# Kernel optimization log

Hardware: AMD Instinct MI355X
Metric: run time of the kernel (lower is better)

The kernel has to match this reference:

```python
import jax, jax.numpy as jnp
import numpy as np

H, D_MODEL, LEN_Q, LEN_K, D_K, D_V = 16, 1024, 512, 2048, 64, 64
B = 4

def setup_inputs() -> dict:
    key = jax.random.key(0)
    ks = jax.random.split(key, 16)
    s = 0.02
    return {
        "Q": jax.random.normal(ks[0], (B, LEN_Q, D_MODEL), jnp.float32),
        "K": jax.random.normal(ks[1], (B, LEN_K, D_MODEL), jnp.float32),
        "V": jax.random.normal(ks[2], (B, LEN_K, D_MODEL), jnp.float32),
        "node_num": LEN_Q,
        "mask": jax.random.randint(ks[3], (B, LEN_K), 0, 2, jnp.int32),
        # params (stored as [in, out] so y = x @ W + b)
        "Wq": jax.random.normal(ks[4], (D_MODEL, H * D_K), jnp.float32) * s,
        "bq": jnp.zeros((H * D_K,), jnp.float32),
        "Wk": jax.random.normal(ks[5], (D_MODEL, H * D_K), jnp.float32) * s,
        "bk": jnp.zeros((H * D_K,), jnp.float32),
        "Wv": jax.random.normal(ks[6], (D_MODEL, H * D_V), jnp.float32) * s,
        "bv": jnp.zeros((H * D_V,), jnp.float32),
        "Wo": jax.random.normal(ks[7], (H * D_V, D_MODEL), jnp.float32) * s,
        "bo": jnp.zeros((D_MODEL,), jnp.float32),
        "gamma": jnp.ones((D_MODEL,), jnp.float32),
        "beta": jnp.zeros((D_MODEL,), jnp.float32),
    }

def _layernorm(x, gamma, beta, eps=1e-5):
    mu = jnp.mean(x, axis=-1, keepdims=True)
    var = jnp.mean((x - mu) ** 2, axis=-1, keepdims=True)
    return (x - mu) * jax.lax.rsqrt(var + eps) * gamma + beta

def reference(Q, K, V, node_num, mask, Wq, bq, Wk, bk, Wv, bv, Wo, bo, gamma, beta):
    b, lq, _ = Q.shape
    lk = K.shape[1]
    q = (Q @ Wq + bq).reshape(b, lq, H, D_K)   # [B, Lq, h, dk]
    k = (K @ Wk + bk).reshape(b, lk, H, D_K)   # [B, Lk, h, dk]
    v = (V @ Wv + bv).reshape(b, lk, H, D_V)   # [B, Lk, h, dv]
    scores = jnp.einsum('bqhd,bkhd->bhqk', q, k) / jnp.sqrt(jnp.float32(D_K))
    scores = jnp.where(mask[:, None, None, :] == 0, -jnp.inf, scores)
    alpha = jax.nn.softmax(scores, axis=-1)    # [B, h, Lq, Lk]
    out = jnp.einsum('bhqk,bkhd->bqhd', alpha, v).reshape(b, lq, H * D_V)
    out = out @ Wo + bo + Q                    # dropout is identity (eval)
    return _layernorm(out, gamma, beta)
```

## Files before the change

kernel.cpp:

```cpp
#include <hip/hip_runtime.h>

typedef __attribute__((ext_vector_type(8))) __bf16 bf16x8;
typedef __attribute__((ext_vector_type(4))) float f32x4;
typedef __attribute__((ext_vector_type(8))) unsigned short u16x8;

__device__ __forceinline__ float bf2f(unsigned short h) {
  union { unsigned int u; float f; } a; a.u = ((unsigned int)h) << 16; return a.f;
}
__device__ __forceinline__ unsigned short f2bf(float f) {
  __bf16 h = (__bf16)f;
  unsigned short u; __builtin_memcpy(&u, &h, 2); return u;
}
__device__ __forceinline__ float fast_exp2(float x) {
#if __has_builtin(__builtin_amdgcn_exp2f)
  return __builtin_amdgcn_exp2f(x);
#else
  return exp2f(x);
#endif
}
__device__ __forceinline__ bf16x8 ld_frag(const unsigned short* p) {
  bf16x8 r; __builtin_memcpy(&r, p, 16); return r;
}
__device__ __forceinline__ void cp16(unsigned short* dst, const unsigned short* src) {
  u16x8 t; __builtin_memcpy(&t, src, 16); __builtin_memcpy(dst, &t, 16);
}

#if __has_builtin(__builtin_amdgcn_global_load_lds)
typedef __attribute__((address_space(3))) unsigned int lds_u32;
typedef const __attribute__((address_space(1))) unsigned int glb_u32;
__device__ __forceinline__ void gload16(const unsigned short* g, unsigned short* l) {
  __builtin_amdgcn_global_load_lds((glb_u32*)g, (lds_u32*)l, 16, 0, 0);
}
#else
__device__ __forceinline__ void gload16(const unsigned short* g, unsigned short* l) {
  cp16(l, g);
}
#endif


__global__ __launch_bounds__(256) void prep_kernel(
    const float* __restrict__ Q, const float* __restrict__ K, const float* __restrict__ V,
    const float* __restrict__ w0, const float* __restrict__ w1,
    const float* __restrict__ w2, const float* __restrict__ w3,
    unsigned short* __restrict__ qb, unsigned short* __restrict__ kb,
    unsigned short* __restrict__ vb, unsigned short* __restrict__ wt)
{
  __shared__ unsigned short tile[64 * 65];
  const int bid = blockIdx.x;
  const int t = threadIdx.x;
  if (bid < 9216) {
    const float* in; unsigned short* out; int i;
    if (bid < 1024)      { in = Q; out = qb; i = bid * 256 + t; }
    else if (bid < 5120) { in = K; out = kb; i = (bid - 1024) * 256 + t; }
    else                 { in = V; out = vb; i = (bid - 5120) * 256 + t; }
    float tf[8]; __builtin_memcpy(tf, &in[(size_t)i * 8], 32);
    unsigned short tu[8];
#pragma unroll
    for (int j = 0; j < 8; j++) tu[j] = f2bf(tf[j]);
    __builtin_memcpy(&out[(size_t)i * 8], tu, 16);
    return;
  }
  const int t4 = bid - 9216;
  const int z = t4 >> 8;
  const float* in = (z == 0) ? w0 : (z == 1) ? w1 : (z == 2) ? w2 : w3;
  unsigned short* o = wt + (size_t)z * 1048576;
  const int dim = 1024;
  const int n0 = (t4 & 15) * 64, k0 = ((t4 >> 4) & 15) * 64;
#pragma unroll
  for (int e = 0; e < 16; e++) {
    int idx = e * 256 + t;
    int i = idx >> 6, j = idx & 63;
    tile[i * 65 + j] = f2bf(in[(size_t)(k0 + i) * dim + n0 + j]);
  }
  __syncthreads();
#pragma unroll
  for (int e = 0; e < 16; e++) {
    int idx = e * 256 + t;
    int i = idx >> 6, j = idx & 63;
    o[(size_t)(n0 + i) * dim + k0 + j] = tile[j * 65 + i];
  }
}

__global__ __launch_bounds__(256, 4) void projqk_kernel(
    const unsigned short* __restrict__ qb,
    const unsigned short* __restrict__ kb,
    const unsigned short* __restrict__ WT4,
    const float* __restrict__ bq, const float* __restrict__ bk,
    unsigned short* __restrict__ qp,
    unsigned short* __restrict__ ktiles)
{
  __shared__ unsigned short pool[18432];
  const int bid = blockIdx.x;
  const int tid  = threadIdx.x;
  const int wave = tid >> 6;
  const int lane = tid & 63;
  const int quad = lane >> 4;
  const int l16  = lane & 15;
  const int K = 1024;
  const f32x4 fz = {0.0f, 0.0f, 0.0f, 0.0f};
  const int srow0 = tid >> 2;
  const int scol  = (tid & 3) * 8;
  const int gcol  = ((tid & 3) ^ ((tid >> 2) & 3)) * 8;
  const int sq    = (quad ^ (l16 & 3)) * 8;
  const int NT = K >> 5;

  if (bid < 512) {
    const int m0 = (bid & 31) * 64;
    const int n0 = (bid >> 5) * 64;
    const int wm = (wave & 1) * 32;
    const int wn = (wave >> 1) * 32;
    f32x4 acc[2][2];
#pragma unroll
    for (int i = 0; i < 2; i++)
#pragma unroll
      for (int j = 0; j < 2; j++) acc[i][j] = fz;

    auto stage = [&](int s, int k0) {
      unsigned short* Asb = pool + s * 2048;
      unsigned short* Bsb = pool + 6144 + s * 2048;
      gload16(&qb[(size_t)(m0 + srow0) * K + k0 + gcol], &Asb[srow0 * 32 + scol]);
      gload16(&WT4[(size_t)(n0 + srow0) * K + k0 + gcol], &Bsb[srow0 * 32 + scol]);
    };
    stage(0, 0);
    stage(1, 32);
    for (int kt = 0; kt < NT; ++kt) {
      if (kt + 1 < NT) asm volatile("s_waitcnt vmcnt(2)" ::: "memory");
      else             asm volatile("s_waitcnt vmcnt(0)" ::: "memory");
      __builtin_amdgcn_s_barrier();
      const int cur = kt % 3;
      const unsigned short* Asb = pool + cur * 2048;
      const unsigned short* Bsb = pool + 6144 + cur * 2048;
      bf16x8 afr[2], bfr[2];
#pragma unroll
      for (int mt = 0; mt < 2; mt++) afr[mt] = ld_frag(&Asb[(wm + mt * 16 + l16) * 32 + sq]);
#pragma unroll
      for (int nt = 0; nt < 2; nt++) bfr[nt] = ld_frag(&Bsb[(wn + nt * 16 + l16) * 32 + sq]);
#pragma unroll
      for (int mt = 0; mt < 2; mt++)
#pragma unroll
        for (int nt = 0; nt < 2; nt++)
          acc[mt][nt] = __builtin_amdgcn_mfma_f32_16x16x32_bf16(afr[mt], bfr[nt], acc[mt][nt], 0, 0, 0);
      if (kt + 2 < NT) stage((kt + 2) % 3, (kt + 2) << 5);
    }
    const float cscale = 0.18033688011112042f;
#pragma unroll
    for (int nt = 0; nt < 2; nt++) {
      int col = n0 + wn + nt * 16 + l16;
      float bsc = bq[col];
#pragma unroll
      for (int mt = 0; mt < 2; mt++) {
        int rowb = m0 + wm + mt * 16 + quad * 4;
#pragma unroll
        for (int r = 0; r < 4; r++)
          qp[(size_t)(rowb + r) * 1024 + col] = f2bf((acc[mt][nt][r] + bsc) * cscale);
      }
    }
  } else {
    const int tb = bid - 512;
    const int m0 = (tb & 63) * 128;
    const int n0 = (tb >> 6) * 64;
    const int wm = (wave & 1) * 64;
    const int wn = (wave >> 1) * 32;
    const unsigned short* BT = WT4 + 1048576;
    f32x4 acc[4][2];
#pragma unroll
    for (int i = 0; i < 4; i++)
#pragma unroll
      for (int j = 0; j < 2; j++) acc[i][j] = fz;

    const int srow1 = srow0 + 64;
    auto stage = [&](int s, int k0) {
      unsigned short* Asb = pool + s * 4096;
      unsigned short* Bsb = pool + 12288 + s * 2048;
      gload16(&kb[(size_t)(m0 + srow0) * K + k0 + gcol], &Asb[srow0 * 32 + scol]);
      gload16(&kb[(size_t)(m0 + srow1) * K + k0 + gcol], &Asb[srow1 * 32 + scol]);
      gload16(&BT[(size_t)(n0 + srow0) * K + k0 + gcol], &Bsb[srow0 * 32 + scol]);
    };
    stage(0, 0);
    stage(1, 32);
    for (int kt = 0; kt < NT; ++kt) {
      if (kt + 1 < NT) asm volatile("s_waitcnt vmcnt(3)" ::: "memory");
      else             asm volatile("s_waitcnt vmcnt(0)" ::: "memory");
      __builtin_amdgcn_s_barrier();
      const int cur = kt % 3;
      const unsigned short* Asb = pool + cur * 4096;
      const unsigned short* Bsb = pool + 12288 + cur * 2048;
      bf16x8 afr[4], bfr[2];
#pragma unroll
      for (int mt = 0; mt < 4; mt++) afr[mt] = ld_frag(&Asb[(wm + mt * 16 + l16) * 32 + sq]);
#pragma unroll
      for (int nt = 0; nt < 2; nt++) bfr[nt] = ld_frag(&Bsb[(wn + nt * 16 + l16) * 32 + sq]);
#pragma unroll
      for (int mt = 0; mt < 4; mt++)
#pragma unroll
        for (int nt = 0; nt < 2; nt++)
          acc[mt][nt] = __builtin_amdgcn_mfma_f32_16x16x32_bf16(afr[mt], bfr[nt], acc[mt][nt], 0, 0, 0);
      if (kt + 2 < NT) stage((kt + 2) % 3, (kt + 2) << 5);
    }
#pragma unroll
    for (int nt = 0; nt < 2; nt++) {
      const int col = n0 + wn + nt * 16 + l16;
      const float bvv = bk[col];
      const int h  = col >> 6;
      const int dk = col & 63;
      const int kc = dk >> 5;
      const int dq = (dk >> 3) & 3;
      const int de = dk & 7;
#pragma unroll
      for (int mt = 0; mt < 4; mt++) {
#pragma unroll
        for (int r = 0; r < 4; r++) {
          const int row = m0 + wm + mt * 16 + quad * 4 + r;
          const int bb = row >> 11, key = row & 2047;
          const size_t tile = ((size_t)((bb * 16 + h) * 32 + (key >> 6))) * 4096;
          const int knt = (key & 63) >> 4;
          const int kl16 = key & 15;
          ktiles[tile + ((size_t)((knt * 2 + kc) * 64 + dq * 16 + kl16)) * 8 + de] =
              f2bf(acc[mt][nt][r] + bvv);
        }
      }
    }
  }
}

__global__ __launch_bounds__(256) void gemm_bt64_kernel(
    const unsigned short* __restrict__ A,
    const unsigned short* __restrict__ BT,
    const float* __restrict__ bias,
    unsigned short* __restrict__ C,
    int M, int N, int K, float cscale)
{
  __shared__ unsigned short pool[12288];
  const int tid  = threadIdx.x;
  const int wave = tid >> 6;
  const int lane = tid & 63;
  const int quad = lane >> 4;
  const int l16  = lane & 15;
  const int m0 = blockIdx.x * 64;
  const int n0 = blockIdx.y * 64;
  const int wm = (wave & 1) * 32;
  const int wn = (wave >> 1) * 32;

  const f32x4 fz = {0.0f, 0.0f, 0.0f, 0.0f};
  f32x4 acc[2][2];
#pragma unroll
  for (int i = 0; i < 2; i++)
#pragma unroll
    for (int j = 0; j < 2; j++) acc[i][j] = fz;

  const int srow0 = tid >> 2;
  const int scol  = (tid & 3) * 8;
  const int gcol  = ((tid & 3) ^ ((tid >> 2) & 3)) * 8;
  const int sq    = (quad ^ (l16 & 3)) * 8;

  auto stage = [&](int s, int k0) {
    unsigned short* Asb = pool + s * 2048;
    unsigned short* Bsb = pool + 6144 + s * 2048;
    gload16(&A[(size_t)(m0 + srow0) * K + k0 + gcol], &Asb[srow0 * 32 + scol]);
    gload16(&BT[(size_t)(n0 + srow0) * K + k0 + gcol], &Bsb[srow0 * 32 + scol]);
  };

  const int NT = K >> 5;
  stage(0, 0);
  stage(1, 32);
  for (int kt = 0; kt < NT; ++kt) {
    if (kt + 1 < NT) asm volatile("s_waitcnt vmcnt(2)" ::: "memory");
    else             asm volatile("s_waitcnt vmcnt(0)" ::: "memory");
    __builtin_amdgcn_s_barrier();
    const int cur = kt % 3;
    const unsigned short* Asb = pool + cur * 2048;
    const unsigned short* Bsb = pool + 6144 + cur * 2048;
    bf16x8 afr[2], bfr[2];
#pragma unroll
    for (int mt = 0; mt < 2; mt++) afr[mt] = ld_frag(&Asb[(wm + mt * 16 + l16) * 32 + sq]);
#pragma unroll
    for (int nt = 0; nt < 2; nt++) bfr[nt] = ld_frag(&Bsb[(wn + nt * 16 + l16) * 32 + sq]);
#pragma unroll
    for (int mt = 0; mt < 2; mt++)
#pragma unroll
      for (int nt = 0; nt < 2; nt++)
        acc[mt][nt] = __builtin_amdgcn_mfma_f32_16x16x32_bf16(afr[mt], bfr[nt], acc[mt][nt], 0, 0, 0);
    if (kt + 2 < NT) stage((kt + 2) % 3, (kt + 2) << 5);
  }

#pragma unroll
  for (int nt = 0; nt < 2; nt++) {
    int col = n0 + wn + nt * 16 + l16;
    float bsc = bias[col];
#pragma unroll
    for (int mt = 0; mt < 2; mt++) {
      int rowb = m0 + wm + mt * 16 + quad * 4;
#pragma unroll
      for (int r = 0; r < 4; r++)
        C[(size_t)(rowb + r) * N + col] = f2bf((acc[mt][nt][r] + bsc) * cscale);
    }
  }
}

__global__ __launch_bounds__(256, 4) void gemm_vt_kernel(
    const unsigned short* __restrict__ A,
    const unsigned short* __restrict__ BT,
    const float* __restrict__ bias,
    unsigned short* __restrict__ vt)
{
  __shared__ unsigned short pool[18432];
  const int K = 1024;
  const int tid  = threadIdx.x;
  const int wave = tid >> 6;
  const int lane = tid & 63;
  const int quad = lane >> 4;
  const int l16  = lane & 15;
  const int m0 = blockIdx.x * 128;
  const int n0 = blockIdx.y * 64;
  const int wm = (wave & 1) * 64;
  const int wn = (wave >> 1) * 32;

  const f32x4 fz = {0.0f, 0.0f, 0.0f, 0.0f};
  f32x4 acc[4][2];
#pragma unroll
  for (int i = 0; i < 4; i++)
#pragma unroll
    for (int j = 0; j < 2; j++) acc[i][j] = fz;

  const int srow0 = tid >> 2;
  const int srow1 = srow0 + 64;
  const int scol  = (tid & 3) * 8;
  const int gcol  = ((tid & 3) ^ ((tid >> 2) & 3)) * 8;
  const int sq    = (quad ^ (l16 & 3)) * 8;

  auto stage = [&](int s, int k0) {
    unsigned short* Asb = pool + s * 4096;
    unsigned short* Bsb = pool + 12288 + s * 2048;
    gload16(&A[(size_t)(m0 + srow0) * K + k0 + gcol], &Asb[srow0 * 32 + scol]);
    gload16(&A[(size_t)(m0 + srow1) * K + k0 + gcol], &Asb[srow1 * 32 + scol]);
    gload16(&BT[(size_t)(n0 + srow0) * K + k0 + gcol], &Bsb[srow0 * 32 + scol]);
  };

  const int NT = K >> 5;
  stage(0, 0);
  stage(1, 32);
  for (int kt = 0; kt < NT; ++kt) {
    if (kt + 1 < NT) asm volatile("s_waitcnt vmcnt(3)" ::: "memory");
    else             asm volatile("s_waitcnt vmcnt(0)" ::: "memory");
    __builtin_amdgcn_s_barrier();
    const int cur = kt % 3;
    const unsigned short* Asb = pool + cur * 4096;
    const unsigned short* Bsb = pool + 12288 + cur * 2048;
    bf16x8 afr[4], bfr[2];
#pragma unroll
    for (int mt = 0; mt < 4; mt++) afr[mt] = ld_frag(&Asb[(wm + mt * 16 + l16) * 32 + sq]);
#pragma unroll
    for (int nt = 0; nt < 2; nt++) bfr[nt] = ld_frag(&Bsb[(wn + nt * 16 + l16) * 32 + sq]);
#pragma unroll
    for (int mt = 0; mt < 4; mt++)
#pragma unroll
      for (int nt = 0; nt < 2; nt++)
        acc[mt][nt] = __builtin_amdgcn_mfma_f32_16x16x32_bf16(afr[mt], bfr[nt], acc[mt][nt], 0, 0, 0);
    if (kt + 2 < NT) stage((kt + 2) % 3, (kt + 2) << 5);
  }
  __syncthreads();

  unsigned short* Ts = pool + wave * 2304;
#pragma unroll
  for (int nt = 0; nt < 2; nt++) {
    const float bvv = bias[n0 + wn + nt * 16 + l16];
#pragma unroll
    for (int mt = 0; mt < 4; mt++)
#pragma unroll
      for (int r = 0; r < 4; r++)
        Ts[(nt * 16 + l16) * 72 + mt * 16 + quad * 4 + r] = f2bf(acc[mt][nt][r] + bvv);
  }
  {
    const int R0 = m0 + wm;
    const int b  = R0 >> 11;
    const int ktile = (R0 & 2047) >> 6;
    const int h = n0 >> 6;
    const int dv_local = lane >> 1;
    const int kc = lane & 1;
    const int dv = wn + dv_local;
    const int dvt = dv >> 4, vl16 = dv & 15;
    const size_t vtile = ((size_t)((b * 16 + h) * 32 + ktile)) * 4096;
#pragma unroll
    for (int jb = 0; jb < 4; jb++) {
      const size_t dst = vtile + ((size_t)((dvt * 2 + kc) * 64 + jb * 16 + vl16)) * 8;
      cp16((unsigned short*)&vt[dst], &Ts[dv_local * 72 + kc * 32 + jb * 8]);
    }
  }
}

__global__ __launch_bounds__(512) void attn_kernel(
    const unsigned short* __restrict__ qp,
    const unsigned short* __restrict__ kp,
    const unsigned short* __restrict__ vt,
    const int* __restrict__ mask,
    unsigned short* __restrict__ attn)
{
  __shared__ unsigned short Kb[3][4096];
  __shared__ unsigned short Vb[3][4096];
  __shared__ int Ms[2048];
  __shared__ unsigned short Ps[8][16 * 72];

  const int tid  = threadIdx.x;
  const int wave = tid >> 6;
  const int lane = tid & 63;
  const int quad = lane >> 4;
  const int l16  = lane & 15;
  const int bid  = blockIdx.x;
  const int bh = bid & 63;
  const int qg = bid >> 6;
  const int b = bh >> 4, h = bh & 15;

  bf16x8 aq[2];
  {
    const size_t qbase = ((size_t)(b * 512 + qg * 128 + wave * 16 + l16)) * 1024 + h * 64;
#pragma unroll
    for (int kc = 0; kc < 2; kc++)
      aq[kc] = ld_frag(&qp[qbase + kc * 32 + quad * 8]);
  }
  {
    const unsigned short* mg = (const unsigned short*)(mask + b * 2048);
    unsigned short* ml = (unsigned short*)Ms;
    gload16(mg + tid * 8, ml + tid * 8);
  }
  asm volatile("s_waitcnt vmcnt(0)" ::: "memory");

  const size_t kvbase = (size_t)bh * 131072;
  auto stageKV = [&](int s, int kt) {
    const unsigned short* ksrc = kp + kvbase + (size_t)kt * 4096;
    const unsigned short* vsrc = vt + kvbase + (size_t)kt * 4096;
    gload16(ksrc + tid * 8, &Kb[s][tid * 8]);
    gload16(vsrc + tid * 8, &Vb[s][tid * 8]);
  };

  const f32x4 fz = {0.0f, 0.0f, 0.0f, 0.0f};
  float l_i[4];
  f32x4 O[4];
#pragma unroll
  for (int r = 0; r < 4; r++) { l_i[r] = 0.0f; O[r] = fz; }

  stageKV(0, 0);
  stageKV(1, 1);
  for (int kt = 0; kt < 32; ++kt) {
    if (kt + 1 < 32) asm volatile("s_waitcnt vmcnt(2)" ::: "memory");
    else             asm volatile("s_waitcnt vmcnt(0)" ::: "memory");
    __builtin_amdgcn_s_barrier();
    const int cur = kt % 3;

    int mk[4];
#pragma unroll
    for (int nt = 0; nt < 4; nt++) mk[nt] = Ms[kt * 64 + nt * 16 + l16];

    f32x4 s[4];
#pragma unroll
    for (int nt = 0; nt < 4; nt++) s[nt] = fz;
    __builtin_amdgcn_s_setprio(1);
#pragma unroll
    for (int nt = 0; nt < 4; nt++)
#pragma unroll
      for (int kc = 0; kc < 2; kc++) {
        bf16x8 bk = ld_frag(&Kb[cur][(nt * 2 + kc) * 512 + lane * 8]);
        s[nt] = __builtin_amdgcn_mfma_f32_16x16x32_bf16(aq[kc], bk, s[nt], 0, 0, 0);
      }
    __builtin_amdgcn_s_setprio(0);

#pragma unroll
    for (int nt = 0; nt < 4; nt++) {
      bool ok = (mk[nt] != 0);
#pragma unroll
      for (int r = 0; r < 4; r++) {
        float p = ok ? fast_exp2(s[nt][r]) : 0.0f;
        l_i[r] += p;
        Ps[wave][(quad * 4 + r) * 72 + nt * 16 + l16] = f2bf(p);
      }
    }

    bf16x8 ap[2];
#pragma unroll
    for (int kc = 0; kc < 2; kc++)
      ap[kc] = ld_frag(&Ps[wave][l16 * 72 + kc * 32 + quad * 8]);
    __builtin_amdgcn_s_setprio(1);
#pragma unroll
    for (int dvt = 0; dvt < 4; dvt++)
#pragma unroll
      for (int kc = 0; kc < 2; kc++) {
        bf16x8 bvf = ld_frag(&Vb[cur][(dvt * 2 + kc) * 512 + lane * 8]);
        O[dvt] = __builtin_amdgcn_mfma_f32_16x16x32_bf16(ap[kc], bvf, O[dvt], 0, 0, 0);
      }
    __builtin_amdgcn_s_setprio(0);
    if (kt + 2 < 32) stageKV((kt + 2) % 3, kt + 2);
  }

#pragma unroll
  for (int off = 1; off < 16; off <<= 1)
#pragma unroll
    for (int r = 0; r < 4; r++) l_i[r] += __shfl_xor(l_i[r], off);

  const int growb = b * 512 + qg * 128 + wave * 16 + quad * 4;
#pragma unroll
  for (int r = 0; r < 4; r++) {
    const float inv = (l_i[r] > 0.0f) ? (1.0f / l_i[r]) : 0.0f;
#pragma unroll
    for (int dvt = 0; dvt < 4; dvt++)
      attn[(size_t)(growb + r) * 1024 + h * 64 + dvt * 16 + l16] = f2bf(O[dvt][r] * inv);
  }
}

__global__ __launch_bounds__(256) void ln_kernel(
    const unsigned short* __restrict__ x,
    const float* __restrict__ resid,
    const float* __restrict__ gamma,
    const float* __restrict__ beta,
    float* __restrict__ out)
{
  const int row = blockIdx.x;
  const int t = threadIdx.x;
  const int wave = t >> 6, lane = t & 63;
  __shared__ float red[8];
  float v[4];
  float s1 = 0.0f, s2 = 0.0f;
#pragma unroll
  for (int i = 0; i < 4; i++) {
    int e = t + i * 256;
    float val = bf2f(x[(size_t)row * 1024 + e]) + resid[(size_t)row * 1024 + e];
    v[i] = val; s1 += val; s2 += val * val;
  }
#pragma unroll
  for (int off = 1; off < 64; off <<= 1) { s1 += __shfl_xor(s1, off); s2 += __shfl_xor(s2, off); }
  if (lane == 0) { red[wave] = s1; red[4 + wave] = s2; }
  __syncthreads();
  s1 = red[0] + red[1] + red[2] + red[3];
  s2 = red[4] + red[5] + red[6] + red[7];
  float mu  = s1 * (1.0f / 1024.0f);
  float var = s2 * (1.0f / 1024.0f) - mu * mu;
  float rstd = rsqrtf(var + 1e-5f);
#pragma unroll
  for (int i = 0; i < 4; i++) {
    int e = t + i * 256;
    out[(size_t)row * 1024 + e] = (v[i] - mu) * rstd * gamma[e] + beta[e];
  }
}

extern "C" void kernel_launch(void* const* d_in, const int* in_sizes, int n_in,
                              void* d_out, int out_size, void* d_ws, size_t ws_size,
                              hipStream_t stream) {
  (void)out_size; (void)ws_size;
  const float* Q = (const float*)d_in[0];
  const float* K = (const float*)d_in[1];
  const float* V = (const float*)d_in[2];

  int ix = 3;
  if (ix < n_in && in_sizes[ix] == 1) ix++;
  const int* mask  = (const int*)d_in[ix++];
  const float* Wq = (const float*)d_in[ix++]; const float* bq = (const float*)d_in[ix++];
  const float* Wk = (const float*)d_in[ix++]; const float* bk = (const float*)d_in[ix++];
  const float* Wv = (const float*)d_in[ix++]; const float* bv = (const float*)d_in[ix++];
  const float* Wo = (const float*)d_in[ix++]; const float* bo = (const float*)d_in[ix++];
  const float* gm = (const float*)d_in[ix++]; const float* bt = (const float*)d_in[ix++];

  char* ws = (char*)d_ws;
  dim3 blk(256);
  dim3 blk512(512);

  unsigned short* WT4    = (unsigned short*)(ws);
  unsigned short* qp     = (unsigned short*)(ws + (8ull  << 20));
  unsigned short* kb     = (unsigned short*)(ws + (12ull << 20));
  unsigned short* vtiles = kb;
  unsigned short* vb     = (unsigned short*)(ws + (28ull << 20));
  unsigned short* qb     = (unsigned short*)(ws + (44ull << 20));
  unsigned short* at     = qb;
  unsigned short* ktiles = (unsigned short*)(ws + (48ull << 20));

  prep_kernel<<<dim3(10240), blk, 0, stream>>>(Q, K, V, Wq, Wk, Wv, Wo, qb, kb, vb, WT4);
  projqk_kernel<<<dim3(1536), blk, 0, stream>>>(qb, kb, WT4, bq, bk, qp, ktiles);
  gemm_vt_kernel<<<dim3(64, 16), blk, 0, stream>>>(vb, WT4 + 2097152, bv, vtiles);
  attn_kernel<<<dim3(256), blk512, 0, stream>>>(qp, ktiles, vtiles, mask, at);
  gemm_bt64_kernel<<<dim3(32, 16), blk, 0, stream>>>(at, WT4 + 3145728, bo, qp, 2048, 1024, 1024, 1.0f);
  ln_kernel<<<dim3(2048), blk, 0, stream>>>(qp, Q, gm, bt, (float*)d_out);
}
```

Baseline: 259.9 us.

## Fuse fp32-to-bf16 activation conversion into projection GEMM loads and merge V projection

Drops the separate pass that converts Q, K and V from fp32 to bf16. The projection GEMMs now load fp32 activations into registers, convert them and store bf16 into LDS, while the weight tile still uses direct global-to-LDS loads. The V projection is merged into the same launch as the Q and K projections. This removes a full write and reread of the bf16 activation copies and one kernel launch, in exchange for register-staged loads, more VGPR pressure, and loss of the XOR swizzle on LDS fragment reads, which may cause bank conflicts.

```diff
diff --git a/kernel.cpp b/kernel.cpp
--- a/kernel.cpp
+++ b/kernel.cpp
@@ -37,30 +37,14 @@
 }
 #endif
 
-
 __global__ __launch_bounds__(256) void prep_kernel(
-    const float* __restrict__ Q, const float* __restrict__ K, const float* __restrict__ V,
     const float* __restrict__ w0, const float* __restrict__ w1,
     const float* __restrict__ w2, const float* __restrict__ w3,
-    unsigned short* __restrict__ qb, unsigned short* __restrict__ kb,
-    unsigned short* __restrict__ vb, unsigned short* __restrict__ wt)
+    unsigned short* __restrict__ wt)
 {
   __shared__ unsigned short tile[64 * 65];
-  const int bid = blockIdx.x;
+  const int t4 = blockIdx.x;
   const int t = threadIdx.x;
-  if (bid < 9216) {
-    const float* in; unsigned short* out; int i;
-    if (bid < 1024)      { in = Q; out = qb; i = bid * 256 + t; }
-    else if (bid < 5120) { in = K; out = kb; i = (bid - 1024) * 256 + t; }
-    else                 { in = V; out = vb; i = (bid - 5120) * 256 + t; }
-    float tf[8]; __builtin_memcpy(tf, &in[(size_t)i * 8], 32);
-    unsigned short tu[8];
-#pragma unroll
-    for (int j = 0; j < 8; j++) tu[j] = f2bf(tf[j]);
-    __builtin_memcpy(&out[(size_t)i * 8], tu, 16);
-    return;
-  }
-  const int t4 = bid - 9216;
   const int z = t4 >> 8;
   const float* in = (z == 0) ? w0 : (z == 1) ? w1 : (z == 2) ? w2 : w3;
   unsigned short* o = wt + (size_t)z * 1048576;
@@ -81,13 +65,13 @@
   }
 }
 
-__global__ __launch_bounds__(256, 4) void projqk_kernel(
-    const unsigned short* __restrict__ qb,
-    const unsigned short* __restrict__ kb,
+__global__ __launch_bounds__(256, 4) void proj_kernel(
+    const float* __restrict__ Qf, const float* __restrict__ Kf, const float* __restrict__ Vf,
     const unsigned short* __restrict__ WT4,
-    const float* __restrict__ bq, const float* __restrict__ bk,
+    const float* __restrict__ bq, const float* __restrict__ bk, const float* __restrict__ bv,
     unsigned short* __restrict__ qp,
-    unsigned short* __restrict__ ktiles)
+    unsigned short* __restrict__ ktiles,
+    unsigned short* __restrict__ vtiles)
 {
   __shared__ unsigned short pool[18432];
   const int bid = blockIdx.x;
@@ -96,108 +80,131 @@
   const int lane = tid & 63;
   const int quad = lane >> 4;
   const int l16  = lane & 15;
-  const int K = 1024;
+  const int KD = 1024, NT = 32;
   const f32x4 fz = {0.0f, 0.0f, 0.0f, 0.0f};
   const int srow0 = tid >> 2;
   const int scol  = (tid & 3) * 8;
-  const int gcol  = ((tid & 3) ^ ((tid >> 2) & 3)) * 8;
-  const int sq    = (quad ^ (l16 & 3)) * 8;
-  const int NT = K >> 5;
+
+#define Q_ISSUE(kt, X0, X1) do { \
+    const int k0_ = (kt) << 5; \
+    gload16(&BT[(size_t)(n0 + srow0) * KD + k0_ + scol], &pool[6144 + ((kt) % 3) * 2048 + srow0 * 32 + scol]); \
+    __builtin_memcpy(&X0, &Qf[(size_t)(m0 + srow0) * KD + k0_ + scol], 16); \
+    __builtin_memcpy(&X1, &Qf[(size_t)(m0 + srow0) * KD + k0_ + scol + 4], 16); \
+  } while (0)
+#define Q_COMMIT(slot, X0, X1) do { \
+    unsigned short tu_[8]; \
+    for (int j_ = 0; j_ < 4; j_++) { tu_[j_] = f2bf(X0[j_]); tu_[4 + j_] = f2bf(X1[j_]); } \
+    __builtin_memcpy(&pool[(slot) * 2048 + srow0 * 32 + scol], tu_, 16); \
+  } while (0)
+#define Q_COMP(kt) do { \
+    const unsigned short* Asb_ = pool + ((kt) % 3) * 2048; \
+    const unsigned short* Bsb_ = pool + 6144 + ((kt) % 3) * 2048; \
+    bf16x8 afr_[2], bfr_[2]; \
+    for (int mt_ = 0; mt_ < 2; mt_++) afr_[mt_] = ld_frag(&Asb_[(wm + mt_ * 16 + l16) * 32 + quad * 8]); \
+    for (int nt_ = 0; nt_ < 2; nt_++) bfr_[nt_] = ld_frag(&Bsb_[(wn + nt_ * 16 + l16) * 32 + quad * 8]); \
+    for (int mt_ = 0; mt_ < 2; mt_++) \
+      for (int nt_ = 0; nt_ < 2; nt_++) \
+        acc[mt_][nt_] = __builtin_amdgcn_mfma_f32_16x16x32_bf16(afr_[mt_], bfr_[nt_], acc[mt_][nt_], 0, 0, 0); \
+  } while (0)
+#define Q_ITER(kt, I0, I1, C0, C1) do { \
+    __builtin_amdgcn_s_barrier(); \
+    Q_COMP(kt); \
+    if ((kt) + 2 < NT) Q_ISSUE((kt) + 2, I0, I1); \
+    if ((kt) + 1 < NT) { \
+      if ((kt) + 2 < NT) { asm volatile("s_waitcnt vmcnt(3)" ::: "memory"); } \
+      else               { asm volatile("s_waitcnt vmcnt(0)" ::: "memory"); } \
+      Q_COMMIT(((kt) + 1) % 3, C0, C1); \
+      asm volatile("s_waitcnt lgkmcnt(0)" ::: "memory"); \
+    } \
+  } while (0)
+
+#define KV_ISSUE(AP, kt, X0, X1, X2, X3) do { \
+    const int k0_ = (kt) << 5; \
+    gload16(&BT[(size_t)(n0 + srow0) * KD + k0_ + scol], &pool[12288 + ((kt) % 3) * 2048 + srow0 * 32 + scol]); \
+    __builtin_memcpy(&X0, &AP[(size_t)(m0 + srow0) * KD + k0_ + scol], 16); \
+    __builtin_memcpy(&X1, &AP[(size_t)(m0 + srow0) * KD + k0_ + scol + 4], 16); \
+    __builtin_memcpy(&X2, &AP[(size_t)(m0 + srow1) * KD + k0_ + scol], 16); \
+    __builtin_memcpy(&X3, &AP[(size_t)(m0 + srow1) * KD + k0_ + scol + 4], 16); \
+  } while (0)
+#define KV_COMMIT(slot, X0, X1, X2, X3) do { \
+    unsigned short tu_[8]; \
+    for (int j_ = 0; j_ < 4; j_++) { tu_[j_] = f2bf(X0[j_]); tu_[4 + j_] = f2bf(X1[j_]); } \
+    __builtin_memcpy(&pool[(slot) * 4096 + srow0 * 32 + scol], tu_, 16); \
+    for (int j_ = 0; j_ < 4; j_++) { tu_[j_] = f2bf(X2[j_]); tu_[4 + j_] = f2bf(X3[j_]); } \
+    __builtin_memcpy(&pool[(slot) * 4096 + srow1 * 32 + scol], tu_, 16); \
+  } while (0)
+#define KV_COMP(kt) do { \
+    const unsigned short* Asb_ = pool + ((kt) % 3) * 4096; \
+    const unsigned short* Bsb_ = pool + 12288 + ((kt) % 3) * 2048; \
+    bf16x8 afr_[4], bfr_[2]; \
+    for (int mt_ = 0; mt_ < 4; mt_++) afr_[mt_] = ld_frag(&Asb_[(wm + mt_ * 16 + l16) * 32 + quad * 8]); \
+    for (int nt_ = 0; nt_ < 2; nt_++) bfr_[nt_] = ld_frag(&Bsb_[(wn + nt_ * 16 + l16) * 32 + quad * 8]); \
+    for (int mt_ = 0; mt_ < 4; mt_++) \
+      for (int nt_ = 0; nt_ < 2; nt_++) \
+        acc[mt_][nt_] = __builtin_amdgcn_mfma_f32_16x16x32_bf16(afr_[mt_], bfr_[nt_], acc[mt_][nt_], 0, 0, 0); \
+  } while (0)
+#define KV_ITER(AP, kt, I0, I1, I2, I3, C0, C1, C2, C3) do { \
+    __builtin_amdgcn_s_barrier(); \
+    KV_COMP(kt); \
+    if ((kt) + 2 < NT) KV_ISSUE(AP, (kt) + 2, I0, I1, I2, I3); \
+    if ((kt) + 1 < NT) { \
+      if ((kt) + 2 < NT) { asm volatile("s_waitcnt vmcnt(5)" ::: "memory"); } \
+      else               { asm volatile("s_waitcnt vmcnt(0)" ::: "memory"); } \
+      KV_COMMIT(((kt) + 1) % 3, C0, C1, C2, C3); \
+      asm volatile("s_waitcnt lgkmcnt(0)" ::: "memory"); \
+    } \
+  } while (0)
 
   if (bid < 512) {
     const int m0 = (bid & 31) * 64;
     const int n0 = (bid >> 5) * 64;
     const int wm = (wave & 1) * 32;
     const int wn = (wave >> 1) * 32;
+    const unsigned short* BT = WT4;
     f32x4 acc[2][2];
-#pragma unroll
     for (int i = 0; i < 2; i++)
-#pragma unroll
       for (int j = 0; j < 2; j++) acc[i][j] = fz;
-
-    auto stage = [&](int s, int k0) {
-      unsigned short* Asb = pool + s * 2048;
-      unsigned short* Bsb = pool + 6144 + s * 2048;
-      gload16(&qb[(size_t)(m0 + srow0) * K + k0 + gcol], &Asb[srow0 * 32 + scol]);
-      gload16(&WT4[(size_t)(n0 + srow0) * K + k0 + gcol], &Bsb[srow0 * 32 + scol]);
-    };
-    stage(0, 0);
-    stage(1, 32);
-    for (int kt = 0; kt < NT; ++kt) {
-      if (kt + 1 < NT) asm volatile("s_waitcnt vmcnt(2)" ::: "memory");
-      else             asm volatile("s_waitcnt vmcnt(0)" ::: "memory");
-      __builtin_amdgcn_s_barrier();
-      const int cur = kt % 3;
-      const unsigned short* Asb = pool + cur * 2048;
-      const unsigned short* Bsb = pool + 6144 + cur * 2048;
-      bf16x8 afr[2], bfr[2];
-#pragma unroll
-      for (int mt = 0; mt < 2; mt++) afr[mt] = ld_frag(&Asb[(wm + mt * 16 + l16) * 32 + sq]);
-#pragma unroll
-      for (int nt = 0; nt < 2; nt++) bfr[nt] = ld_frag(&Bsb[(wn + nt * 16 + l16) * 32 + sq]);
-#pragma unroll
-      for (int mt = 0; mt < 2; mt++)
-#pragma unroll
-        for (int nt = 0; nt < 2; nt++)
-          acc[mt][nt] = __builtin_amdgcn_mfma_f32_16x16x32_bf16(afr[mt], bfr[nt], acc[mt][nt], 0, 0, 0);
-      if (kt + 2 < NT) stage((kt + 2) % 3, (kt + 2) << 5);
+    f32x4 qa0, qa1, qb0, qb1;
+    Q_ISSUE(0, qa0, qa1);
+    Q_ISSUE(1, qb0, qb1);
+    asm volatile("s_waitcnt vmcnt(3)" ::: "memory");
+    Q_COMMIT(0, qa0, qa1);
+    asm volatile("s_waitcnt lgkmcnt(0)" ::: "memory");
+    for (int kt = 0; kt < NT; kt += 2) {
+      Q_ITER(kt,     qa0, qa1, qb0, qb1);
+      Q_ITER(kt + 1, qb0, qb1, qa0, qa1);
     }
     const float cscale = 0.18033688011112042f;
-#pragma unroll
     for (int nt = 0; nt < 2; nt++) {
       int col = n0 + wn + nt * 16 + l16;
       float bsc = bq[col];
-#pragma unroll
       for (int mt = 0; mt < 2; mt++) {
         int rowb = m0 + wm + mt * 16 + quad * 4;
-#pragma unroll
         for (int r = 0; r < 4; r++)
           qp[(size_t)(rowb + r) * 1024 + col] = f2bf((acc[mt][nt][r] + bsc) * cscale);
       }
     }
-  } else {
+  } else if (bid < 1536) {
     const int tb = bid - 512;
     const int m0 = (tb & 63) * 128;
     const int n0 = (tb >> 6) * 64;
     const int wm = (wave & 1) * 64;
     const int wn = (wave >> 1) * 32;
+    const int srow1 = srow0 + 64;
     const unsigned short* BT = WT4 + 1048576;
     f32x4 acc[4][2];
-#pragma unroll
     for (int i = 0; i < 4; i++)
-#pragma unroll
       for (int j = 0; j < 2; j++) acc[i][j] = fz;
-
-    const int srow1 = srow0 + 64;
-    auto stage = [&](int s, int k0) {
-      unsigned short* Asb = pool + s * 4096;
-      unsigned short* Bsb = pool + 12288 + s * 2048;
-      gload16(&kb[(size_t)(m0 + srow0) * K + k0 + gcol], &Asb[srow0 * 32 + scol]);
-      gload16(&kb[(size_t)(m0 + srow1) * K + k0 + gcol], &Asb[srow1 * 32 + scol]);
-      gload16(&BT[(size_t)(n0 + srow0) * K + k0 + gcol], &Bsb[srow0 * 32 + scol]);
-    };
-    stage(0, 0);
-    stage(1, 32);
-    for (int kt = 0; kt < NT; ++kt) {
-      if (kt + 1 < NT) asm volatile("s_waitcnt vmcnt(3)" ::: "memory");
-      else             asm volatile("s_waitcnt vmcnt(0)" ::: "memory");
-      __builtin_amdgcn_s_barrier();
-      const int cur = kt % 3;
-      const unsigned short* Asb = pool + cur * 4096;
-      const unsigned short* Bsb = pool + 12288 + cur * 2048;
-      bf16x8 afr[4], bfr[2];
-#pragma unroll
-      for (int mt = 0; mt < 4; mt++) afr[mt] = ld_frag(&Asb[(wm + mt * 16 + l16) * 32 + sq]);
-#pragma unroll
-      for (int nt = 0; nt < 2; nt++) bfr[nt] = ld_frag(&Bsb[(wn + nt * 16 + l16) * 32 + sq]);
-#pragma unroll
-      for (int mt = 0; mt < 4; mt++)
-#pragma unroll
-        for (int nt = 0; nt < 2; nt++)
-          acc[mt][nt] = __builtin_amdgcn_mfma_f32_16x16x32_bf16(afr[mt], bfr[nt], acc[mt][nt], 0, 0, 0);
-      if (kt + 2 < NT) stage((kt + 2) % 3, (kt + 2) << 5);
-    }
-#pragma unroll
+    f32x4 ka0, ka1, ka2, ka3, kb0, kb1, kb2, kb3;
+    KV_ISSUE(Kf, 0, ka0, ka1, ka2, ka3);
+    KV_ISSUE(Kf, 1, kb0, kb1, kb2, kb3);
+    asm volatile("s_waitcnt vmcnt(5)" ::: "memory");
+    KV_COMMIT(0, ka0, ka1, ka2, ka3);
+    asm volatile("s_waitcnt lgkmcnt(0)" ::: "memory");
+    for (int kt = 0; kt < NT; kt += 2) {
+      KV_ITER(Kf, kt,     ka0, ka1, ka2, ka3, kb0, kb1, kb2, kb3);
+      KV_ITER(Kf, kt + 1, kb0, kb1, kb2, kb3, ka0, ka1, ka2, ka3);
+    }
     for (int nt = 0; nt < 2; nt++) {
       const int col = n0 + wn + nt * 16 + l16;
       const float bvv = bk[col];
@@ -206,9 +213,7 @@
       const int kc = dk >> 5;
       const int dq = (dk >> 3) & 3;
       const int de = dk & 7;
-#pragma unroll
       for (int mt = 0; mt < 4; mt++) {
-#pragma unroll
         for (int r = 0; r < 4; r++) {
           const int row = m0 + wm + mt * 16 + quad * 4 + r;
           const int bb = row >> 11, key = row & 2047;
@@ -220,7 +225,60 @@
         }
       }
     }
-  }
+  } else {
+    const int tb = bid - 1536;
+    const int m0 = (tb & 63) * 128;
+    const int n0 = (tb >> 6) * 64;
+    const int wm = (wave & 1) * 64;
+    const int wn = (wave >> 1) * 32;
+    const int srow1 = srow0 + 64;
+    const unsigned short* BT = WT4 + 2097152;
+    f32x4 acc[4][2];
+    for (int i = 0; i < 4; i++)
+      for (int j = 0; j < 2; j++) acc[i][j] = fz;
+    f32x4 va0, va1, va2, va3, vb0, vb1, vb2, vb3;
+    KV_ISSUE(Vf, 0, va0, va1, va2, va3);
+    KV_ISSUE(Vf, 1, vb0, vb1, vb2, vb3);
+    asm volatile("s_waitcnt vmcnt(5)" ::: "memory");
+    KV_COMMIT(0, va0, va1, va2, va3);
+    asm volatile("s_waitcnt lgkmcnt(0)" ::: "memory");
+    for (int kt = 0; kt < NT; kt += 2) {
+      KV_ITER(Vf, kt,     va0, va1, va2, va3, vb0, vb1, vb2, vb3);
+      KV_ITER(Vf, kt + 1, vb0, vb1, vb2, vb3, va0, va1, va2, va3);
+    }
+    __syncthreads();
+
+    unsigned short* Ts = pool + wave * 2304;
+    for (int nt = 0; nt < 2; nt++) {
+      const float bvv = bv[n0 + wn + nt * 16 + l16];
+      for (int mt = 0; mt < 4; mt++)
+        for (int r = 0; r < 4; r++)
+          Ts[(nt * 16 + l16) * 72 + mt * 16 + quad * 4 + r] = f2bf(acc[mt][nt][r] + bvv);
+    }
+    {
+      const int R0 = m0 + wm;
+      const int b  = R0 >> 11;
+      const int ktile = (R0 & 2047) >> 6;
+      const int h = n0 >> 6;
+      const int dv_local = lane >> 1;
+      const int kc = lane & 1;
+      const int dv = wn + dv_local;
+      const int dvt = dv >> 4, vl16 = dv & 15;
+      const size_t vtile = ((size_t)((b * 16 + h) * 32 + ktile)) * 4096;
+      for (int jb = 0; jb < 4; jb++) {
+        const size_t dst = vtile + ((size_t)((dvt * 2 + kc) * 64 + jb * 16 + vl16)) * 8;
+        cp16((unsigned short*)&vtiles[dst], &Ts[dv_local * 72 + kc * 32 + jb * 8]);
+      }
+    }
+  }
+#undef Q_ISSUE
+#undef Q_COMMIT
+#undef Q_COMP
+#undef Q_ITER
+#undef KV_ISSUE
+#undef KV_COMMIT
+#undef KV_COMP
+#undef KV_ITER
 }
 
 __global__ __launch_bounds__(256) void gemm_bt64_kernel(
@@ -297,97 +355,6 @@
   }
 }
 
-__global__ __launch_bounds__(256, 4) void gemm_vt_kernel(
-    const unsigned short* __restrict__ A,
-    const unsigned short* __restrict__ BT,
-    const float* __restrict__ bias,
-    unsigned short* __restrict__ vt)
-{
-  __shared__ unsigned short pool[18432];
-  const int K = 1024;
-  const int tid  = threadIdx.x;
-  const int wave = tid >> 6;
-  const int lane = tid & 63;
-  const int quad = lane >> 4;
-  const int l16  = lane & 15;
-  const int m0 = blockIdx.x * 128;
-  const int n0 = blockIdx.y * 64;
-  const int wm = (wave & 1) * 64;
-  const int wn = (wave >> 1) * 32;
-
-  const f32x4 fz = {0.0f, 0.0f, 0.0f, 0.0f};
-  f32x4 acc[4][2];
-#pragma unroll
-  for (int i = 0; i < 4; i++)
-#pragma unroll
-    for (int j = 0; j < 2; j++) acc[i][j] = fz;
-
-  const int srow0 = tid >> 2;
-  const int srow1 = srow0 + 64;
-  const int scol  = (tid & 3) * 8;
-  const int gcol  = ((tid & 3) ^ ((tid >> 2) & 3)) * 8;
-  const int sq    = (quad ^ (l16 & 3)) * 8;
-
-  auto stage = [&](int s, int k0) {
-    unsigned short* Asb = pool + s * 4096;
-    unsigned short* Bsb = pool + 12288 + s * 2048;
-    gload16(&A[(size_t)(m0 + srow0) * K + k0 + gcol], &Asb[srow0 * 32 + scol]);
-    gload16(&A[(size_t)(m0 + srow1) * K + k0 + gcol], &Asb[srow1 * 32 + scol]);
-    gload16(&BT[(size_t)(n0 + srow0) * K + k0 + gcol], &Bsb[srow0 * 32 + scol]);
-  };
-
-  const int NT = K >> 5;
-  stage(0, 0);
-  stage(1, 32);
-  for (int kt = 0; kt < NT; ++kt) {
-    if (kt + 1 < NT) asm volatile("s_waitcnt vmcnt(3)" ::: "memory");
-    else             asm volatile("s_waitcnt vmcnt(0)" ::: "memory");
-    __builtin_amdgcn_s_barrier();
-    const int cur = kt % 3;
-    const unsigned short* Asb = pool + cur * 4096;
-    const unsigned short* Bsb = pool + 12288 + cur * 2048;
-    bf16x8 afr[4], bfr[2];
-#pragma unroll
-    for (int mt = 0; mt < 4; mt++) afr[mt] = ld_frag(&Asb[(wm + mt * 16 + l16) * 32 + sq]);
-#pragma unroll
-    for (int nt = 0; nt < 2; nt++) bfr[nt] = ld_frag(&Bsb[(wn + nt * 16 + l16) * 32 + sq]);
-#pragma unroll
-    for (int mt = 0; mt < 4; mt++)
-#pragma unroll
-      for (int nt = 0; nt < 2; nt++)
-        acc[mt][nt] = __builtin_amdgcn_mfma_f32_16x16x32_bf16(afr[mt], bfr[nt], acc[mt][nt], 0, 0, 0);
-    if (kt + 2 < NT) stage((kt + 2) % 3, (kt + 2) << 5);
-  }
-  __syncthreads();
-
-  unsigned short* Ts = pool + wave * 2304;
-#pragma unroll
-  for (int nt = 0; nt < 2; nt++) {
-    const float bvv = bias[n0 + wn + nt * 16 + l16];
-#pragma unroll
-    for (int mt = 0; mt < 4; mt++)
-#pragma unroll
-      for (int r = 0; r < 4; r++)
-        Ts[(nt * 16 + l16) * 72 + mt * 16 + quad * 4 + r] = f2bf(acc[mt][nt][r] + bvv);
-  }
-  {
-    const int R0 = m0 + wm;
-    const int b  = R0 >> 11;
-    const int ktile = (R0 & 2047) >> 6;
-    const int h = n0 >> 6;
-    const int dv_local = lane >> 1;
-    const int kc = lane & 1;
-    const int dv = wn + dv_local;
-    const int dvt = dv >> 4, vl16 = dv & 15;
-    const size_t vtile = ((size_t)((b * 16 + h) * 32 + ktile)) * 4096;
-#pragma unroll
-    for (int jb = 0; jb < 4; jb++) {
-      const size_t dst = vtile + ((size_t)((dvt * 2 + kc) * 64 + jb * 16 + vl16)) * 8;
-      cp16((unsigned short*)&vt[dst], &Ts[dv_local * 72 + kc * 32 + jb * 8]);
-    }
-  }
-}
-
 __global__ __launch_bounds__(512) void attn_kernel(
     const unsigned short* __restrict__ qp,
     const unsigned short* __restrict__ kp,
@@ -563,16 +530,12 @@
 
   unsigned short* WT4    = (unsigned short*)(ws);
   unsigned short* qp     = (unsigned short*)(ws + (8ull  << 20));
-  unsigned short* kb     = (unsigned short*)(ws + (12ull << 20));
-  unsigned short* vtiles = kb;
-  unsigned short* vb     = (unsigned short*)(ws + (28ull << 20));
-  unsigned short* qb     = (unsigned short*)(ws + (44ull << 20));
-  unsigned short* at     = qb;
-  unsigned short* ktiles = (unsigned short*)(ws + (48ull << 20));
-
-  prep_kernel<<<dim3(10240), blk, 0, stream>>>(Q, K, V, Wq, Wk, Wv, Wo, qb, kb, vb, WT4);
-  projqk_kernel<<<dim3(1536), blk, 0, stream>>>(qb, kb, WT4, bq, bk, qp, ktiles);
-  gemm_vt_kernel<<<dim3(64, 16), blk, 0, stream>>>(vb, WT4 + 2097152, bv, vtiles);
+  unsigned short* ktiles = (unsigned short*)(ws + (12ull << 20));
+  unsigned short* vtiles = (unsigned short*)(ws + (28ull << 20));
+  unsigned short* at     = (unsigned short*)(ws + (44ull << 20));
+
+  prep_kernel<<<dim3(1024), blk, 0, stream>>>(Wq, Wk, Wv, Wo, WT4);
+  proj_kernel<<<dim3(2560), blk, 0, stream>>>(Q, K, V, WT4, bq, bk, bv, qp, ktiles, vtiles);
   attn_kernel<<<dim3(256), blk512, 0, stream>>>(qp, ktiles, vtiles, mask, at);
   gemm_bt64_kernel<<<dim3(32, 16), blk, 0, stream>>>(at, WT4 + 3145728, bo, qp, 2048, 1024, 1024, 1.0f);
   ln_kernel<<<dim3(2048), blk, 0, stream>>>(qp, Q, gm, bt, (float*)d_out);
```

After: 275.6 us. +6.1%, slower.

## Give each wave private LDS staging to drop block barriers in projection GEMMs

Applied to the files above, without the earlier changes.

The Q/K projection and V projection GEMMs now have each wave load its own A and B sub-tiles into a private LDS region, so the per-iteration block-wide s_barrier is removed and each wave waits only on its own vmcnt. This removes cross-wave synchronisation stalls in the k-loop. The cost is duplicated global loads, since waves sharing rows or columns each fetch them, plus doubled LDS per block, which lowers the occupancy hint from 4 to 2. The XOR swizzle is also dropped, so LDS bank conflicts may increase.

```diff
diff --git a/kernel.cpp b/kernel.cpp
--- a/kernel.cpp
+++ b/kernel.cpp
@@ -36,7 +36,6 @@
   cp16(l, g);
 }
 #endif
-
 
 __global__ __launch_bounds__(256) void prep_kernel(
     const float* __restrict__ Q, const float* __restrict__ K, const float* __restrict__ V,
@@ -81,7 +80,7 @@
   }
 }
 
-__global__ __launch_bounds__(256, 4) void projqk_kernel(
+__global__ __launch_bounds__(256, 2) void projqk_kernel(
     const unsigned short* __restrict__ qb,
     const unsigned short* __restrict__ kb,
     const unsigned short* __restrict__ WT4,
@@ -89,20 +88,18 @@
     unsigned short* __restrict__ qp,
     unsigned short* __restrict__ ktiles)
 {
-  __shared__ unsigned short pool[18432];
+  __shared__ unsigned short pool[36864];
   const int bid = blockIdx.x;
   const int tid  = threadIdx.x;
   const int wave = tid >> 6;
   const int lane = tid & 63;
   const int quad = lane >> 4;
   const int l16  = lane & 15;
-  const int K = 1024;
+  const int KD = 1024, NT = 32;
   const f32x4 fz = {0.0f, 0.0f, 0.0f, 0.0f};
-  const int srow0 = tid >> 2;
-  const int scol  = (tid & 3) * 8;
-  const int gcol  = ((tid & 3) ^ ((tid >> 2) & 3)) * 8;
-  const int sq    = (quad ^ (l16 & 3)) * 8;
-  const int NT = K >> 5;
+  const int wbase = wave * 9216;
+  const int r0 = lane >> 2;
+  const int c0 = (lane & 3) * 8;
 
   if (bid < 512) {
     const int m0 = (bid & 31) * 64;
@@ -116,25 +113,25 @@
       for (int j = 0; j < 2; j++) acc[i][j] = fz;
 
     auto stage = [&](int s, int k0) {
-      unsigned short* Asb = pool + s * 2048;
-      unsigned short* Bsb = pool + 6144 + s * 2048;
-      gload16(&qb[(size_t)(m0 + srow0) * K + k0 + gcol], &Asb[srow0 * 32 + scol]);
-      gload16(&WT4[(size_t)(n0 + srow0) * K + k0 + gcol], &Bsb[srow0 * 32 + scol]);
+      unsigned short* wA = pool + wbase + s * 2048;
+      unsigned short* wB = wA + 1024;
+      gload16(&qb[(size_t)(m0 + wm + r0) * KD + k0 + c0],       wA + lane * 8);
+      gload16(&qb[(size_t)(m0 + wm + 16 + r0) * KD + k0 + c0],  wA + 512 + lane * 8);
+      gload16(&WT4[(size_t)(n0 + wn + r0) * KD + k0 + c0],      wB + lane * 8);
+      gload16(&WT4[(size_t)(n0 + wn + 16 + r0) * KD + k0 + c0], wB + 512 + lane * 8);
     };
     stage(0, 0);
     stage(1, 32);
     for (int kt = 0; kt < NT; ++kt) {
-      if (kt + 1 < NT) asm volatile("s_waitcnt vmcnt(2)" ::: "memory");
+      if (kt + 1 < NT) asm volatile("s_waitcnt vmcnt(4)" ::: "memory");
       else             asm volatile("s_waitcnt vmcnt(0)" ::: "memory");
-      __builtin_amdgcn_s_barrier();
-      const int cur = kt % 3;
-      const unsigned short* Asb = pool + cur * 2048;
-      const unsigned short* Bsb = pool + 6144 + cur * 2048;
+      const unsigned short* wA = pool + wbase + (kt % 3) * 2048;
+      const unsigned short* wB = wA + 1024;
       bf16x8 afr[2], bfr[2];
 #pragma unroll
-      for (int mt = 0; mt < 2; mt++) afr[mt] = ld_frag(&Asb[(wm + mt * 16 + l16) * 32 + sq]);
-#pragma unroll
-      for (int nt = 0; nt < 2; nt++) bfr[nt] = ld_frag(&Bsb[(wn + nt * 16 + l16) * 32 + sq]);
+      for (int mt = 0; mt < 2; mt++) afr[mt] = ld_frag(&wA[(mt * 16 + l16) * 32 + quad * 8]);
+#pragma unroll
+      for (int nt = 0; nt < 2; nt++) bfr[nt] = ld_frag(&wB[(nt * 16 + l16) * 32 + quad * 8]);
 #pragma unroll
       for (int mt = 0; mt < 2; mt++)
 #pragma unroll
@@ -168,28 +165,28 @@
 #pragma unroll
       for (int j = 0; j < 2; j++) acc[i][j] = fz;
 
-    const int srow1 = srow0 + 64;
     auto stage = [&](int s, int k0) {
-      unsigned short* Asb = pool + s * 4096;
-      unsigned short* Bsb = pool + 12288 + s * 2048;
-      gload16(&kb[(size_t)(m0 + srow0) * K + k0 + gcol], &Asb[srow0 * 32 + scol]);
-      gload16(&kb[(size_t)(m0 + srow1) * K + k0 + gcol], &Asb[srow1 * 32 + scol]);
-      gload16(&BT[(size_t)(n0 + srow0) * K + k0 + gcol], &Bsb[srow0 * 32 + scol]);
+      unsigned short* wA = pool + wbase + s * 3072;
+      unsigned short* wB = wA + 2048;
+      gload16(&kb[(size_t)(m0 + wm + r0) * KD + k0 + c0],       wA + lane * 8);
+      gload16(&kb[(size_t)(m0 + wm + 16 + r0) * KD + k0 + c0],  wA + 512 + lane * 8);
+      gload16(&kb[(size_t)(m0 + wm + 32 + r0) * KD + k0 + c0],  wA + 1024 + lane * 8);
+      gload16(&kb[(size_t)(m0 + wm + 48 + r0) * KD + k0 + c0],  wA + 1536 + lane * 8);
+      gload16(&BT[(size_t)(n0 + wn + r0) * KD + k0 + c0],       wB + lane * 8);
+      gload16(&BT[(size_t)(n0 + wn + 16 + r0) * KD + k0 + c0],  wB + 512 + lane * 8);
     };
     stage(0, 0);
     stage(1, 32);
     for (int kt = 0; kt < NT; ++kt) {
-      if (kt + 1 < NT) asm volatile("s_waitcnt vmcnt(3)" ::: "memory");
+      if (kt + 1 < NT) asm volatile("s_waitcnt vmcnt(6)" ::: "memory");
       else             asm volatile("s_waitcnt vmcnt(0)" ::: "memory");
-      __builtin_amdgcn_s_barrier();
-      const int cur = kt % 3;
-      const unsigned short* Asb = pool + cur * 4096;
-      const unsigned short* Bsb = pool + 12288 + cur * 2048;
+      const unsigned short* wA = pool + wbase + (kt % 3) * 3072;
+      const unsigned short* wB = wA + 2048;
       bf16x8 afr[4], bfr[2];
 #pragma unroll
-      for (int mt = 0; mt < 4; mt++) afr[mt] = ld_frag(&Asb[(wm + mt * 16 + l16) * 32 + sq]);
-#pragma unroll
-      for (int nt = 0; nt < 2; nt++) bfr[nt] = ld_frag(&Bsb[(wn + nt * 16 + l16) * 32 + sq]);
+      for (int mt = 0; mt < 4; mt++) afr[mt] = ld_frag(&wA[(mt * 16 + l16) * 32 + quad * 8]);
+#pragma unroll
+      for (int nt = 0; nt < 2; nt++) bfr[nt] = ld_frag(&wB[(nt * 16 + l16) * 32 + quad * 8]);
 #pragma unroll
       for (int mt = 0; mt < 4; mt++)
 #pragma unroll
@@ -219,6 +216,92 @@
               f2bf(acc[mt][nt][r] + bvv);
         }
       }
+    }
+  }
+}
+
+__global__ __launch_bounds__(256, 2) void gemm_vt_kernel(
+    const unsigned short* __restrict__ A,
+    const unsigned short* __restrict__ BT,
+    const float* __restrict__ bias,
+    unsigned short* __restrict__ vt)
+{
+  __shared__ unsigned short pool[36864];
+  const int KD = 1024, NT = 32;
+  const int tid  = threadIdx.x;
+  const int wave = tid >> 6;
+  const int lane = tid & 63;
+  const int quad = lane >> 4;
+  const int l16  = lane & 15;
+  const int m0 = blockIdx.x * 128;
+  const int n0 = blockIdx.y * 64;
+  const int wm = (wave & 1) * 64;
+  const int wn = (wave >> 1) * 32;
+  const int wbase = wave * 9216;
+  const int r0 = lane >> 2;
+  const int c0 = (lane & 3) * 8;
+
+  const f32x4 fz = {0.0f, 0.0f, 0.0f, 0.0f};
+  f32x4 acc[4][2];
+#pragma unroll
+  for (int i = 0; i < 4; i++)
+#pragma unroll
+    for (int j = 0; j < 2; j++) acc[i][j] = fz;
+
+  auto stage = [&](int s, int k0) {
+    unsigned short* wA = pool + wbase + s * 3072;
+    unsigned short* wB = wA + 2048;
+    gload16(&A[(size_t)(m0 + wm + r0) * KD + k0 + c0],       wA + lane * 8);
+    gload16(&A[(size_t)(m0 + wm + 16 + r0) * KD + k0 + c0],  wA + 512 + lane * 8);
+    gload16(&A[(size_t)(m0 + wm + 32 + r0) * KD + k0 + c0],  wA + 1024 + lane * 8);
+    gload16(&A[(size_t)(m0 + wm + 48 + r0) * KD + k0 + c0],  wA + 1536 + lane * 8);
+    gload16(&BT[(size_t)(n0 + wn + r0) * KD + k0 + c0],      wB + lane * 8);
+    gload16(&BT[(size_t)(n0 + wn + 16 + r0) * KD + k0 + c0], wB + 512 + lane * 8);
+  };
+  stage(0, 0);
+  stage(1, 32);
+  for (int kt = 0; kt < NT; ++kt) {
+    if (kt + 1 < NT) asm volatile("s_waitcnt vmcnt(6)" ::: "memory");
+    else             asm volatile("s_waitcnt vmcnt(0)" ::: "memory");
+    const unsigned short* wA = pool + wbase + (kt % 3) * 3072;
+    const unsigned short* wB = wA + 2048;
+    bf16x8 afr[4], bfr[2];
+#pragma unroll
+    for (int mt = 0; mt < 4; mt++) afr[mt] = ld_frag(&wA[(mt * 16 + l16) * 32 + quad * 8]);
+#pragma unroll
+    for (int nt = 0; nt < 2; nt++) bfr[nt] = ld_frag(&wB[(nt * 16 + l16) * 32 + quad * 8]);
+#pragma unroll
+    for (int mt = 0; mt < 4; mt++)
+#pragma unroll
+      for (int nt = 0; nt < 2; nt++)
+        acc[mt][nt] = __builtin_amdgcn_mfma_f32_16x16x32_bf16(afr[mt], bfr[nt], acc[mt][nt], 0, 0, 0);
+    if (kt + 2 < NT) stage((kt + 2) % 3, (kt + 2) << 5);
+  }
+  asm volatile("s_waitcnt lgkmcnt(0)" ::: "memory");
+  unsigned short* Ts = pool + wbase;
+#pragma unroll
+  for (int nt = 0; nt < 2; nt++) {
+    const float bvv = bias[n0 + wn + nt * 16 + l16];
+#pragma unroll
+    for (int mt = 0; mt < 4; mt++)
+#pragma unroll
+      for (int r = 0; r < 4; r++)
+        Ts[(nt * 16 + l16) * 72 + mt * 16 + quad * 4 + r] = f2bf(acc[mt][nt][r] + bvv);
+  }
+  {
+    const int R0 = m0 + wm;
+    const int b  = R0 >> 11;
+    const int ktile = (R0 & 2047) >> 6;
+    const int h = n0 >> 6;
+    const int dv_local = lane >> 1;
+    const int kc = lane & 1;
+    const int dv = wn + dv_local;
+    const int dvt = dv >> 4, vl16 = dv & 15;
+    const size_t vtile = ((size_t)((b * 16 + h) * 32 + ktile)) * 4096;
+#pragma unroll
+    for (int jb = 0; jb < 4; jb++) {
+      const size_t dst = vtile + ((size_t)((dvt * 2 + kc) * 64 + jb * 16 + vl16)) * 8;
+      cp16((unsigned short*)&vt[dst], &Ts[dv_local * 72 + kc * 32 + jb * 8]);
     }
   }
 }
@@ -297,97 +380,6 @@
   }
 }
 
-__global__ __launch_bounds__(256, 4) void gemm_vt_kernel(
-    const unsigned short* __restrict__ A,
-    const unsigned short* __restrict__ BT,
-    const float* __restrict__ bias,
-    unsigned short* __restrict__ vt)
-{
-  __shared__ unsigned short pool[18432];
-  const int K = 1024;
-  const int tid  = threadIdx.x;
-  const int wave = tid >> 6;
-  const int lane = tid & 63;
-  const int quad = lane >> 4;
-  const int l16  = lane & 15;
-  const int m0 = blockIdx.x * 128;
-  const int n0 = blockIdx.y * 64;
-  const int wm = (wave & 1) * 64;
-  const int wn = (wave >> 1) * 32;
-
-  const f32x4 fz = {0.0f, 0.0f, 0.0f, 0.0f};
-  f32x4 acc[4][2];
-#pragma unroll
-  for (int i = 0; i < 4; i++)
-#pragma unroll
-    for (int j = 0; j < 2; j++) acc[i][j] = fz;
-
-  const int srow0 = tid >> 2;
-  const int srow1 = srow0 + 64;
-  const int scol  = (tid & 3) * 8;
-  const int gcol  = ((tid & 3) ^ ((tid >> 2) & 3)) * 8;
-  const int sq    = (quad ^ (l16 & 3)) * 8;
-
-  auto stage = [&](int s, int k0) {
-    unsigned short* Asb = pool + s * 4096;
-    unsigned short* Bsb = pool + 12288 + s * 2048;
-    gload16(&A[(size_t)(m0 + srow0) * K + k0 + gcol], &Asb[srow0 * 32 + scol]);
-    gload16(&A[(size_t)(m0 + srow1) * K + k0 + gcol], &Asb[srow1 * 32 + scol]);
-    gload16(&BT[(size_t)(n0 + srow0) * K + k0 + gcol], &Bsb[srow0 * 32 + scol]);
-  };
-
-  const int NT = K >> 5;
-  stage(0, 0);
-  stage(1, 32);
-  for (int kt = 0; kt < NT; ++kt) {
-    if (kt + 1 < NT) asm volatile("s_waitcnt vmcnt(3)" ::: "memory");
-    else             asm volatile("s_waitcnt vmcnt(0)" ::: "memory");
-    __builtin_amdgcn_s_barrier();
-    const int cur = kt % 3;
-    const unsigned short* Asb = pool + cur * 4096;
-    const unsigned short* Bsb = pool + 12288 + cur * 2048;
-    bf16x8 afr[4], bfr[2];
-#pragma unroll
-    for (int mt = 0; mt < 4; mt++) afr[mt] = ld_frag(&Asb[(wm + mt * 16 + l16) * 32 + sq]);
-#pragma unroll
-    for (int nt = 0; nt < 2; nt++) bfr[nt] = ld_frag(&Bsb[(wn + nt * 16 + l16) * 32 + sq]);
-#pragma unroll
-    for (int mt = 0; mt < 4; mt++)
-#pragma unroll
-      for (int nt = 0; nt < 2; nt++)
-        acc[mt][nt] = __builtin_amdgcn_mfma_f32_16x16x32_bf16(afr[mt], bfr[nt], acc[mt][nt], 0, 0, 0);
-    if (kt + 2 < NT) stage((kt + 2) % 3, (kt + 2) << 5);
-  }
-  __syncthreads();
-
-  unsigned short* Ts = pool + wave * 2304;
-#pragma unroll
-  for (int nt = 0; nt < 2; nt++) {
-    const float bvv = bias[n0 + wn + nt * 16 + l16];
-#pragma unroll
-    for (int mt = 0; mt < 4; mt++)
-#pragma unroll
-      for (int r = 0; r < 4; r++)
-        Ts[(nt * 16 + l16) * 72 + mt * 16 + quad * 4 + r] = f2bf(acc[mt][nt][r] + bvv);
-  }
-  {
-    const int R0 = m0 + wm;
-    const int b  = R0 >> 11;
-    const int ktile = (R0 & 2047) >> 6;
-    const int h = n0 >> 6;
-    const int dv_local = lane >> 1;
-    const int kc = lane & 1;
-    const int dv = wn + dv_local;
-    const int dvt = dv >> 4, vl16 = dv & 15;
-    const size_t vtile = ((size_t)((b * 16 + h) * 32 + ktile)) * 4096;
-#pragma unroll
-    for (int jb = 0; jb < 4; jb++) {
-      const size_t dst = vtile + ((size_t)((dvt * 2 + kc) * 64 + jb * 16 + vl16)) * 8;
-      cp16((unsigned short*)&vt[dst], &Ts[dv_local * 72 + kc * 32 + jb * 8]);
-    }
-  }
-}
-
 __global__ __launch_bounds__(512) void attn_kernel(
     const unsigned short* __restrict__ qp,
     const unsigned short* __restrict__ kp,
```

Result: slower. 283.4 us (+9.1%).
